# Kernel tuning notes

Measured on AMD Instinct MI355X. Metric: run time of the kernel, lower is better.

The kernel has to match this reference:

```python
import jax, jax.numpy as jnp
import numpy as np

DN = ('NCHW', 'OIHW', 'NCHW')

def _conv(x, w, b):
    y = jax.lax.conv_general_dilated(x, w, (2, 2), 'SAME', dimension_numbers=DN)
    return jax.nn.relu(y + b[None, :, None, None])

def setup_inputs() -> dict:
    key = jax.random.key(0)
    ks = jax.random.split(key, 20)
    B, S, V, D, NC = 64, 128, 32000, 512, 1000
    inp = {}
    inp['images'] = jax.random.normal(ks[0], (B, 3, 224, 224), jnp.float32)
    inp['sequences'] = jax.random.randint(ks[1], (B, S), 0, V)
    inp['lengths'] = jax.random.randint(ks[2], (B,), 1, S + 1)
    inp['lengths_var'] = inp['lengths']
    s = 0.02
    inp['emb'] = jax.random.normal(ks[3], (V, D), jnp.float32) * s
    # SimpleCNN(3): 4 strided conv blocks 3->64->128->256->512, final_dim=512
    chans = [3, 64, 128, 256, 512]
    for i in range(4):
        inp[f'cw{i+1}'] = jax.random.normal(ks[4 + i], (chans[i + 1], chans[i], 3, 3), jnp.float32) * s
        inp[f'cb{i+1}'] = jnp.zeros((chans[i + 1],), jnp.float32)
    inp['rnn_w'] = jax.random.normal(ks[8], (D, D), jnp.float32) * s
    inp['rnn_b'] = jnp.zeros((D,), jnp.float32)
    inp['fc1_w'] = jax.random.normal(ks[9], (D + 512, 512), jnp.float32) * s
    inp['fc1_b'] = jnp.zeros((512,), jnp.float32)
    inp['fc2_w'] = jax.random.normal(ks[10], (512, 512), jnp.float32) * s
    inp['fc2_b'] = jnp.zeros((512,), jnp.float32)
    inp['clf_w'] = jax.random.normal(ks[11], (512, NC), jnp.float32) * s
    inp['clf_b'] = jnp.zeros((NC,), jnp.float32)
    return inp

def reference(images, sequences, lengths, lengths_var, emb, cw1, cb1, cw2, cb2, cw3, cb3, cw4, cb4, rnn_w, rnn_b, fc1_w, fc1_b, fc2_w, fc2_b, clf_w, clf_b):
    B, S = sequences.shape
    # masked mean over valid tokens (replaces the per-sample python loop)
    we = emb[sequences]                                   # [B,S,512]
    mask = (jnp.arange(S)[None, :] < lengths[:, None]).astype(we.dtype)
    batch_means = (we * mask[:, :, None]).sum(1) / lengths.astype(we.dtype)[:, None]
    sent = batch_means @ rnn_w + rnn_b                    # [B,512]
    # SimpleCNN + global avg pool -> [B,512,1,1] -> squeeze
    x = _conv(images, cw1, cb1)
    x = _conv(x, cw2, cb2)
    x = _conv(x, cw3, cb3)
    x = _conv(x, cw4, cb4)
    img = x.mean(axis=(2, 3))                             # [B,512]
    feats = jnp.concatenate([img, sent], axis=1)          # [B,1024]
    h = jax.nn.relu(feats @ fc1_w + fc1_b)
    h = jax.nn.relu(h @ fc2_w + fc2_b)                    # dropout = identity (eval)
    return h @ clf_w + clf_b
```

## Files before the change

### kernel.cpp

```cpp
#include <hip/hip_runtime.h>
#include <hip/hip_bf16.h>
#include <cstddef>
#include <cstdint>

typedef unsigned short u16;
typedef __attribute__((ext_vector_type(8))) short bf16x8;
typedef __attribute__((ext_vector_type(4))) float f32x4;
typedef __attribute__((ext_vector_type(8))) unsigned short u16x8;

static __device__ __forceinline__ u16 f2bf(float x) {
  unsigned u = __float_as_uint(x);
  u += 0x7fffu + ((u >> 16) & 1u);
  return (u16)(u >> 16);
}
static __device__ __forceinline__ float bflo(unsigned u) { return __uint_as_float(u << 16); }
static __device__ __forceinline__ float bfhi(unsigned u) { return __uint_as_float(u & 0xffff0000u); }

static __device__ __forceinline__ void gll16(const u16* g, u16* l) {
  __builtin_amdgcn_global_load_lds(
      (const __attribute__((address_space(1))) void*)g,
      (__attribute__((address_space(3))) void*)l, 16, 0, 0);
}

static __device__ __forceinline__ void halo_store(u16* buf, int H, int W, int C,
                                                  long long i) {
  const int c8n = C >> 3;
  const int c8 = (int)(i % c8n);
  long long rem = i / c8n;
  const int p = (int)(rem % (W + 1 + H));
  const int n = (int)(rem / (W + 1 + H));
  int y, x;
  if (p <= W) { y = H; x = p; } else { y = p - (W + 1); x = W; }
  const u16x8 z = {0, 0, 0, 0, 0, 0, 0, 0};
  *(u16x8*)(buf + (((size_t)n * (H + 1) + y) * (W + 1) + x) * C + c8 * 8) = z;
}
__global__ __launch_bounds__(256) void zero_halo3(u16* __restrict__ A,
                                                  u16* __restrict__ B,
                                                  u16* __restrict__ Cb, int nimg) {
  long long i = (long long)blockIdx.x * 256 + threadIdx.x;
  const long long cA = (long long)nimg * 225 * 8;
  const long long cB = (long long)nimg * 113 * 16;
  const long long cC = (long long)nimg * 57 * 32;
  if (i < cA) { halo_store(A, 112, 112, 64, i); return; }
  i -= cA;
  if (i < cB) { halo_store(B, 56, 56, 128, i); return; }
  i -= cB;
  if (i < cC) halo_store(Cb, 28, 28, 256, i);
}

__global__ __launch_bounds__(256) void conv1_s2(
    const float* __restrict__ in,
    const float* __restrict__ w,
    const float* __restrict__ bias,
    u16* __restrict__ out) {
  __shared__ float sw[64 * 27];
  __shared__ float sb[64];
  __shared__ u16 so[256 * 64];
  const int tid = threadIdx.x;
  if (tid < 64) sb[tid] = bias[tid];
  for (int i = tid; i < 64 * 27; i += 256) sw[i] = w[i];
  __syncthreads();
  const int n = blockIdx.y;
  const int by = blockIdx.x / 7, bx = blockIdx.x % 7;
  const int oy = by * 16 + (tid >> 4), ox = bx * 16 + (tid & 15);
  const float* ibase = in + (size_t)n * 3 * 224 * 224 + (size_t)(2 * oy) * 224 + 2 * ox;
  float v[27];
  #pragma unroll
  for (int c = 0; c < 3; ++c)
    #pragma unroll
    for (int r = 0; r < 3; ++r)
      #pragma unroll
      for (int s = 0; s < 3; ++s) {
        const int iy = 2 * oy + r, ix = 2 * ox + s;
        float x = 0.f;
        if (iy < 224 && ix < 224) x = ibase[(size_t)c * 224 * 224 + r * 224 + s];
        v[c * 9 + r * 3 + s] = x;
      }
  #pragma unroll
  for (int kc = 0; kc < 8; ++kc) {
    u16x8 pack;
    #pragma unroll
    for (int k8 = 0; k8 < 8; ++k8) {
      const int k = kc * 8 + k8;
      float a = sb[k];
      const float* wk = &sw[k * 27];
      #pragma unroll
      for (int t = 0; t < 27; ++t) a = fmaf(v[t], wk[t], a);
      pack[k8] = f2bf(fmaxf(a, 0.f));
    }
    *(u16x8*)&so[(tid * 8 + (kc ^ (tid & 7))) * 8] = pack;
  }
  __syncthreads();
  u16* obase = out + (((size_t)n * 113 + by * 16) * 113 + bx * 16) * 64;
  #pragma unroll
  for (int it = 0; it < 8; ++it) {
    const int row = it * 2 + (tid >> 7);
    const int q = tid & 127;
    const int px = q >> 3, c8 = q & 7;
    const int p = row * 16 + px;
    u16x8 v8 = *(const u16x8*)&so[(p * 8 + (c8 ^ (p & 7))) * 8];
    *(u16x8*)(obase + ((size_t)row * 113 + px) * 64 + c8 * 8) = v8;
  }
}

static __device__ __forceinline__ void pack_one(const float* __restrict__ w,
                                                u16* __restrict__ pw,
                                                int CB, int NB, int C, int idx) {
  const int j = idx & 7;
  const int L = (idx >> 3) & 63;
  int t = idx >> 9;
  const int nbg = t % NB; t /= NB;
  const int cb = t % CB;
  const int tap = t / CB;
  const int n = nbg * 16 + (L & 15);
  const int c = cb * 32 + ((L >> 4) << 3) + j;
  pw[idx] = f2bf(w[((size_t)n * C + c) * 9 + tap]);
}
__global__ __launch_bounds__(256) void pack_all(
    const float* __restrict__ w2, const float* __restrict__ w3,
    const float* __restrict__ w4, u16* __restrict__ p2,
    u16* __restrict__ p3, u16* __restrict__ p4) {
  int i = blockIdx.x * 256 + threadIdx.x;
  if (i < 9 * 64 * 128) { pack_one(w2, p2, 2, 8, 64, i); return; }
  i -= 9 * 64 * 128;
  if (i < 9 * 128 * 256) { pack_one(w3, p3, 4, 16, 128, i); return; }
  i -= 9 * 128 * 256;
  if (i < 9 * 256 * 512) pack_one(w4, p4, 8, 32, 256, i);
}

template<int C, int K, int OH, int OW>
__global__ __launch_bounds__(256) void conv3x3s2_mfma(
    const u16* __restrict__ in,
    const u16* __restrict__ pw,
    const float* __restrict__ bias,
    u16* __restrict__ out) {
  constexpr int IH = 2 * OH, IW = 2 * OW;
  constexpr int PIW = IW + 1;
  constexpr int P = OH * OW;
  constexpr int BM = 128;
  constexpr int MB = (P + BM - 1) / BM;
  constexpr int CB = C / 32, NB = K / 16;
  constexpr int STEPS = 9 * CB;

  __shared__ u16 lds[2][8192];

  const int bm = blockIdx.x % MB;
  const int n = blockIdx.x / MB;
  const int nbh = blockIdx.y;
  const int lane = threadIdx.x & 63, wv = threadIdx.x >> 6;
  const int mh = wv >> 1, nh = wv & 1;

  const u16* ibase = in + (size_t)n * ((IH + 1) * PIW * C);
  int s_abase[4];
  #pragma unroll
  for (int mf = 0; mf < 4; ++mf) {
    int pm = bm * BM + mh * 64 + mf * 16 + (lane & 15);
    int pc = pm < P ? pm : P - 1;
    int oy = pc / OW, ox = pc % OW;
    s_abase[mf] = ((2 * oy) * PIW + 2 * ox) * C + ((lane >> 4) << 3);
  }

  f32x4 acc[4][4];
  #pragma unroll
  for (int mf = 0; mf < 4; ++mf)
    #pragma unroll
    for (int nf = 0; nf < 4; ++nf) acc[mf][nf] = (f32x4){0.f, 0.f, 0.f, 0.f};

  auto STAGE = [&](int st, int buf) {
    if (nh == 0) {
      const int cb = st & (CB - 1);
      const int tap = st / CB;
      const int r = tap / 3, s = tap - 3 * r;
      const int toff = (r * PIW + s) * C + cb * 32;
      #pragma unroll
      for (int mf = 0; mf < 4; ++mf)
        gll16(ibase + s_abase[mf] + toff, &lds[buf][(mh * 4 + mf) * 512]);
    } else {
      const u16* bp = pw + ((size_t)st * NB + nbh * 8 + mh * 4) * 512 + lane * 8;
      #pragma unroll
      for (int nf = 0; nf < 4; ++nf)
        gll16(bp + nf * 512, &lds[buf][4096 + (mh * 4 + nf) * 512]);
    }
  };

  STAGE(0, 0);
  __syncthreads();
  for (int st = 0; st < STEPS; ++st) {
    const int buf = st & 1;
    if (st + 1 < STEPS) STAGE(st + 1, buf ^ 1);
    bf16x8 a[4], b[4];
    #pragma unroll
    for (int mf = 0; mf < 4; ++mf)
      a[mf] = *(const bf16x8*)&lds[buf][(mh * 4 + mf) * 512 + lane * 8];
    #pragma unroll
    for (int nf = 0; nf < 4; ++nf)
      b[nf] = *(const bf16x8*)&lds[buf][4096 + (nh * 4 + nf) * 512 + lane * 8];
    #pragma unroll
    for (int mf = 0; mf < 4; ++mf)
      #pragma unroll
      for (int nf = 0; nf < 4; ++nf)
        acc[mf][nf] = __builtin_amdgcn_mfma_f32_16x16x32_bf16(a[mf], b[nf], acc[mf][nf], 0, 0, 0);
    __syncthreads();
  }

  const int rowg = (lane >> 4) << 2;
  #pragma unroll
  for (int mf = 0; mf < 4; ++mf)
    #pragma unroll
    for (int nf = 0; nf < 4; ++nf) {
      const int ch = (nbh * 8 + nh * 4 + nf) * 16 + (lane & 15);
      const float bv = bias[ch];
      #pragma unroll
      for (int rr = 0; rr < 4; ++rr) {
        const int pix = bm * BM + mh * 64 + mf * 16 + rowg + rr;
        if (pix < P) {
          const int oy = pix / OW, ox = pix % OW;
          out[(((size_t)n * (OH + 1) + oy) * (OW + 1) + ox) * K + ch] =
              f2bf(fmaxf(acc[mf][nf][rr] + bv, 0.f));
        }
      }
    }
}

__global__ __launch_bounds__(256) void avgpool_nhwc(
    const u16* __restrict__ in, float* __restrict__ feats, int n0) {
  const int n = blockIdx.x, t = threadIdx.x;
  const u16* p = in + (size_t)n * (15 * 15 * 512) + t * 2;
  float s0 = 0.f, s1 = 0.f;
  for (int y = 0; y < 14; ++y)
    #pragma unroll
    for (int x = 0; x < 14; ++x) {
      unsigned u = *(const unsigned*)(p + (size_t)(y * 15 + x) * 512);
      s0 += bflo(u);
      s1 += bfhi(u);
    }
  float* f = feats + (size_t)(n0 + n) * 1024;
  f[2 * t] = s0 * (1.f / 196.f);
  f[2 * t + 1] = s1 * (1.f / 196.f);
}

__global__ __launch_bounds__(256) void embed_mean_kernel(
    const int* __restrict__ seq, const int* __restrict__ len,
    const float* __restrict__ emb, float* __restrict__ means) {
  __shared__ float part[3][512];
  const int b = blockIdx.x;
  const int L = len[b];
  const int sg = threadIdx.x >> 6;
  const int d0 = (threadIdx.x & 63) * 8;
  float a[8] = {0.f, 0.f, 0.f, 0.f, 0.f, 0.f, 0.f, 0.f};
  for (int s = sg; s < L; s += 4) {
    const float* e = emb + (size_t)seq[b * 128 + s] * 512 + d0;
    float4 v0 = *(const float4*)e, v1 = *(const float4*)(e + 4);
    a[0] += v0.x; a[1] += v0.y; a[2] += v0.z; a[3] += v0.w;
    a[4] += v1.x; a[5] += v1.y; a[6] += v1.z; a[7] += v1.w;
  }
  if (sg) {
    #pragma unroll
    for (int j = 0; j < 8; ++j) part[sg - 1][d0 + j] = a[j];
  }
  __syncthreads();
  if (sg == 0) {
    const float inv = 1.f / (float)L;
    #pragma unroll
    for (int j = 0; j < 8; ++j)
      means[(size_t)b * 512 + d0 + j] =
          (a[j] + part[0][d0 + j] + part[1][d0 + j] + part[2][d0 + j]) * inv;
  }
}

template<int K, int N, bool RELU>
__global__ __launch_bounds__(256) void fc_kernel(
    const float* __restrict__ x, int ldx,
    const float* __restrict__ w, const float* __restrict__ bias,
    float* __restrict__ out, int ldo) {
  __shared__ float row[2][K];
  const int m0 = blockIdx.y * 2;
  for (int i = threadIdx.x; i < 2 * K; i += 256)
    row[i / K][i % K] = x[(size_t)(m0 + i / K) * ldx + (i % K)];
  __syncthreads();
  const int col = blockIdx.x * 256 + threadIdx.x;
  if (col < N) {
    float acc[2][4] = {{0.f, 0.f, 0.f, 0.f}, {0.f, 0.f, 0.f, 0.f}};
    for (int k = 0; k < K; k += 4) {
      float w0 = w[(size_t)(k + 0) * N + col];
      float w1 = w[(size_t)(k + 1) * N + col];
      float w2 = w[(size_t)(k + 2) * N + col];
      float w3 = w[(size_t)(k + 3) * N + col];
      #pragma unroll
      for (int m = 0; m < 2; ++m) {
        acc[m][0] = fmaf(row[m][k + 0], w0, acc[m][0]);
        acc[m][1] = fmaf(row[m][k + 1], w1, acc[m][1]);
        acc[m][2] = fmaf(row[m][k + 2], w2, acc[m][2]);
        acc[m][3] = fmaf(row[m][k + 3], w3, acc[m][3]);
      }
    }
    const float bv = bias[col];
    #pragma unroll
    for (int m = 0; m < 2; ++m) {
      float a = acc[m][0] + acc[m][1] + acc[m][2] + acc[m][3] + bv;
      out[(size_t)(m0 + m) * ldo + col] = RELU ? fmaxf(a, 0.f) : a;
    }
  }
}

extern "C" void kernel_launch(void* const* d_in, const int* in_sizes, int n_in,
                              void* d_out, int out_size, void* d_ws, size_t ws_size,
                              hipStream_t stream) {
  const float* images = (const float*)d_in[0];
  const int*   seq    = (const int*)d_in[1];
  const int*   len    = (const int*)d_in[2];
  const float* emb    = (const float*)d_in[4];
  const float* cw1 = (const float*)d_in[5];  const float* cb1 = (const float*)d_in[6];
  const float* cw2 = (const float*)d_in[7];  const float* cb2 = (const float*)d_in[8];
  const float* cw3 = (const float*)d_in[9];  const float* cb3 = (const float*)d_in[10];
  const float* cw4 = (const float*)d_in[11]; const float* cb4 = (const float*)d_in[12];
  const float* rnn_w = (const float*)d_in[13]; const float* rnn_b = (const float*)d_in[14];
  const float* fc1_w = (const float*)d_in[15]; const float* fc1_b = (const float*)d_in[16];
  const float* fc2_w = (const float*)d_in[17]; const float* fc2_b = (const float*)d_in[18];
  const float* clf_w = (const float*)d_in[19]; const float* clf_b = (const float*)d_in[20];
  float* out = (float*)d_out;

  const size_t A_E = (size_t)113 * 113 * 64;
  const size_t B_E = (size_t)57 * 57 * 128;
  const size_t C_E = (size_t)29 * 29 * 256;
  const size_t D_E = (size_t)15 * 15 * 512;
  const size_t PW2_E = 9 * 64 * 128, PW3_E = 9 * 128 * 256, PW4_E = 9 * 256 * 512;
  const size_t PER_IMG = (A_E + B_E + C_E + D_E) * 2;
  const size_t FIXED = (PW2_E + PW3_E + PW4_E) * 2 +
                       (size_t)(64 * 512 + 64 * 1024 + 64 * 512 + 64 * 512) * 4;
  int chunk = 64;
  if (ws_size < FIXED + 64 * PER_IMG) {
    size_t avail = (ws_size > FIXED) ? (ws_size - FIXED) : 0;
    size_t c = avail / PER_IMG;
    chunk = (c < 1) ? 1 : (c > 64 ? 64 : (int)c);
  }
  u16* bufA = (u16*)d_ws;
  u16* bufB = bufA + (size_t)chunk * A_E;
  u16* bufC = bufB + (size_t)chunk * B_E;
  u16* bufD = bufC + (size_t)chunk * C_E;
  u16* pw2 = bufD + (size_t)chunk * D_E;
  u16* pw3 = pw2 + PW2_E;
  u16* pw4 = pw3 + PW3_E;
  float* means = (float*)(pw4 + PW4_E);
  float* feats = means + 64 * 512;
  float* h1 = feats + 64 * 1024;
  float* h2 = h1 + 64 * 512;

  {
    const int pk_total = 9 * 64 * 128 + 9 * 128 * 256 + 9 * 256 * 512;
    pack_all<<<(pk_total + 255) / 256, 256, 0, stream>>>(cw2, cw3, cw4, pw2, pw3, pw4);
    long long zt = (long long)chunk * (225 * 8 + 113 * 16 + 57 * 32);
    zero_halo3<<<(int)((zt + 255) / 256), 256, 0, stream>>>(bufA, bufB, bufC, chunk);
  }

  embed_mean_kernel<<<64, 256, 0, stream>>>(seq, len, emb, means);
  fc_kernel<512, 512, false><<<dim3(2, 32), 256, 0, stream>>>(
      means, 512, rnn_w, rnn_b, feats + 512, 1024);

  for (int n0 = 0; n0 < 64; n0 += chunk) {
    int nb = 64 - n0; if (nb > chunk) nb = chunk;
    conv1_s2<<<dim3(49, nb), 256, 0, stream>>>(
        images + (size_t)n0 * 3 * 224 * 224, cw1, cb1, bufA);
    conv3x3s2_mfma<64, 128, 56, 56><<<dim3(25 * nb, 1), 256, 0, stream>>>(
        bufA, pw2, cb2, bufB);
    conv3x3s2_mfma<128, 256, 28, 28><<<dim3(7 * nb, 2), 256, 0, stream>>>(
        bufB, pw3, cb3, bufC);
    conv3x3s2_mfma<256, 512, 14, 14><<<dim3(2 * nb, 4), 256, 0, stream>>>(
        bufC, pw4, cb4, bufD);
    avgpool_nhwc<<<nb, 256, 0, stream>>>(bufD, feats, n0);
  }

  fc_kernel<1024, 512, true ><<<dim3(2, 32), 256, 0, stream>>>(feats, 1024, fc1_w, fc1_b, h1, 512);
  fc_kernel<512,  512, true ><<<dim3(2, 32), 256, 0, stream>>>(h1,    512,  fc2_w, fc2_b, h2, 512);
  fc_kernel<512, 1000, false><<<dim3(4, 32), 256, 0, stream>>>(h2,    512,  clf_w, clf_b, out, 1000);
}
```

Before: 388.2 us.

## Flatten conv M across batch, double K-step depth, and batch more FC rows

The implicit-GEMM conv now tiles the flattened batch×pixel dimension, so partial tiles at image boundaries no longer waste MFMA work. Each pipeline phase now stages two K-steps (BK=64), which halves the number of barriers but doubles LDS to 64 KB per block. The loop also gains setprio hints, explicit waitcnt/barrier scheduling, and launch_bounds(256,2). Separately, the FC kernels process four rows per block instead of two, halving redundant weight reads at the cost of fewer blocks.

```diff
diff --git a/kernel.cpp b/kernel.cpp
--- a/kernel.cpp
+++ b/kernel.cpp
@@ -129,35 +129,35 @@
 }
 
 template<int C, int K, int OH, int OW>
-__global__ __launch_bounds__(256) void conv3x3s2_mfma(
+__global__ __launch_bounds__(256, 2) void conv3x3s2_mfma(
     const u16* __restrict__ in,
     const u16* __restrict__ pw,
     const float* __restrict__ bias,
-    u16* __restrict__ out) {
+    u16* __restrict__ out,
+    int M_total) {
   constexpr int IH = 2 * OH, IW = 2 * OW;
   constexpr int PIW = IW + 1;
   constexpr int P = OH * OW;
-  constexpr int BM = 128;
-  constexpr int MB = (P + BM - 1) / BM;
   constexpr int CB = C / 32, NB = K / 16;
-  constexpr int STEPS = 9 * CB;
-
-  __shared__ u16 lds[2][8192];
-
-  const int bm = blockIdx.x % MB;
-  const int n = blockIdx.x / MB;
+  constexpr int NPH = 9 * CB / 2;
+  static_assert((9 * CB) % 2 == 0, "BK=64 needs even step count");
+
+  __shared__ u16 lds[2][16384];
+
+  const int bm = blockIdx.x;
   const int nbh = blockIdx.y;
   const int lane = threadIdx.x & 63, wv = threadIdx.x >> 6;
   const int mh = wv >> 1, nh = wv & 1;
 
-  const u16* ibase = in + (size_t)n * ((IH + 1) * PIW * C);
-  int s_abase[4];
+  int s_aoff[4];
   #pragma unroll
   for (int mf = 0; mf < 4; ++mf) {
-    int pm = bm * BM + mh * 64 + mf * 16 + (lane & 15);
-    int pc = pm < P ? pm : P - 1;
-    int oy = pc / OW, ox = pc % OW;
-    s_abase[mf] = ((2 * oy) * PIW + 2 * ox) * C + ((lane >> 4) << 3);
+    int pm = bm * 128 + mh * 64 + mf * 16 + (lane & 15);
+    if (pm >= M_total) pm = M_total - 1;
+    const int n = pm / P;
+    const int p = pm - n * P;
+    const int oy = p / OW, ox = p - oy * OW;
+    s_aoff[mf] = ((n * (IH + 1) + 2 * oy) * PIW + 2 * ox) * C + ((lane >> 4) << 3);
   }
 
   f32x4 acc[4][4];
@@ -166,41 +166,63 @@
     #pragma unroll
     for (int nf = 0; nf < 4; ++nf) acc[mf][nf] = (f32x4){0.f, 0.f, 0.f, 0.f};
 
-  auto STAGE = [&](int st, int buf) {
+  auto STAGE = [&](int ph, int buf) {
+    const int st0 = 2 * ph;
+    const int tap = st0 / CB;
+    const int cb0 = st0 & (CB - 1);
+    const int r = tap / 3, s = tap - 3 * r;
+    u16* Lb = &lds[buf][0];
     if (nh == 0) {
-      const int cb = st & (CB - 1);
-      const int tap = st / CB;
-      const int r = tap / 3, s = tap - 3 * r;
-      const int toff = (r * PIW + s) * C + cb * 32;
+      const int toff = (r * PIW + s) * C + cb0 * 32;
+      #pragma unroll
+      for (int kk = 0; kk < 2; ++kk)
+        #pragma unroll
+        for (int mf = 0; mf < 4; ++mf)
+          gll16(in + s_aoff[mf] + toff + kk * 32,
+                &Lb[(kk * 8 + mh * 4 + mf) * 512]);
+    } else {
+      const u16* bp = pw + ((size_t)(st0 + mh) * NB + nbh * 8) * 512 + lane * 8;
+      #pragma unroll
+      for (int nf = 0; nf < 8; ++nf)
+        gll16(bp + nf * 512, &Lb[8192 + (mh * 8 + nf) * 512]);
+    }
+  };
+  auto COMPUTE = [&](int buf) {
+    u16* Lb = &lds[buf][0];
+    bf16x8 a[4][2], b[4][2];
+    #pragma unroll
+    for (int kk = 0; kk < 2; ++kk) {
       #pragma unroll
       for (int mf = 0; mf < 4; ++mf)
-        gll16(ibase + s_abase[mf] + toff, &lds[buf][(mh * 4 + mf) * 512]);
-    } else {
-      const u16* bp = pw + ((size_t)st * NB + nbh * 8 + mh * 4) * 512 + lane * 8;
+        a[mf][kk] = *(const bf16x8*)&Lb[(kk * 8 + mh * 4 + mf) * 512 + lane * 8];
       #pragma unroll
       for (int nf = 0; nf < 4; ++nf)
-        gll16(bp + nf * 512, &lds[buf][4096 + (mh * 4 + nf) * 512]);
-    }
+        b[nf][kk] = *(const bf16x8*)&Lb[8192 + (kk * 8 + nh * 4 + nf) * 512 + lane * 8];
+    }
+    #pragma unroll
+    for (int kk = 0; kk < 2; ++kk)
+      #pragma unroll
+      for (int mf = 0; mf < 4; ++mf)
+        #pragma unroll
+        for (int nf = 0; nf < 4; ++nf)
+          acc[mf][nf] = __builtin_amdgcn_mfma_f32_16x16x32_bf16(
+              a[mf][kk], b[nf][kk], acc[mf][nf], 0, 0, 0);
   };
 
   STAGE(0, 0);
-  __syncthreads();
-  for (int st = 0; st < STEPS; ++st) {
-    const int buf = st & 1;
-    if (st + 1 < STEPS) STAGE(st + 1, buf ^ 1);
-    bf16x8 a[4], b[4];
-    #pragma unroll
-    for (int mf = 0; mf < 4; ++mf)
-      a[mf] = *(const bf16x8*)&lds[buf][(mh * 4 + mf) * 512 + lane * 8];
-    #pragma unroll
-    for (int nf = 0; nf < 4; ++nf)
-      b[nf] = *(const bf16x8*)&lds[buf][4096 + (nh * 4 + nf) * 512 + lane * 8];
-    #pragma unroll
-    for (int mf = 0; mf < 4; ++mf)
-      #pragma unroll
-      for (int nf = 0; nf < 4; ++nf)
-        acc[mf][nf] = __builtin_amdgcn_mfma_f32_16x16x32_bf16(a[mf], b[nf], acc[mf][nf], 0, 0, 0);
-    __syncthreads();
+  asm volatile("s_waitcnt vmcnt(0)" ::: "memory");
+  __builtin_amdgcn_s_barrier();
+  __builtin_amdgcn_sched_barrier(0);
+
+  for (int ph = 0; ph < NPH; ++ph) {
+    const int buf = ph & 1;
+    if (ph + 1 < NPH) STAGE(ph + 1, buf ^ 1);
+    __builtin_amdgcn_s_setprio(1);
+    COMPUTE(buf);
+    __builtin_amdgcn_s_setprio(0);
+    asm volatile("s_waitcnt vmcnt(0)" ::: "memory");
+    __builtin_amdgcn_s_barrier();
+    __builtin_amdgcn_sched_barrier(0);
   }
 
   const int rowg = (lane >> 4) << 2;
@@ -212,9 +234,11 @@
       const float bv = bias[ch];
       #pragma unroll
       for (int rr = 0; rr < 4; ++rr) {
-        const int pix = bm * BM + mh * 64 + mf * 16 + rowg + rr;
-        if (pix < P) {
-          const int oy = pix / OW, ox = pix % OW;
+        const int pm = bm * 128 + mh * 64 + mf * 16 + rowg + rr;
+        if (pm < M_total) {
+          const int n = pm / P;
+          const int p = pm - n * P;
+          const int oy = p / OW, ox = p - oy * OW;
           out[(((size_t)n * (OH + 1) + oy) * (OW + 1) + ox) * K + ch] =
               f2bf(fmaxf(acc[mf][nf][rr] + bv, 0.f));
         }
@@ -273,31 +297,27 @@
     const float* __restrict__ x, int ldx,
     const float* __restrict__ w, const float* __restrict__ bias,
     float* __restrict__ out, int ldo) {
-  __shared__ float row[2][K];
-  const int m0 = blockIdx.y * 2;
-  for (int i = threadIdx.x; i < 2 * K; i += 256)
+  __shared__ float row[4][K];
+  const int m0 = blockIdx.y * 4;
+  for (int i = threadIdx.x; i < 4 * K; i += 256)
     row[i / K][i % K] = x[(size_t)(m0 + i / K) * ldx + (i % K)];
   __syncthreads();
   const int col = blockIdx.x * 256 + threadIdx.x;
   if (col < N) {
-    float acc[2][4] = {{0.f, 0.f, 0.f, 0.f}, {0.f, 0.f, 0.f, 0.f}};
-    for (int k = 0; k < K; k += 4) {
+    float acc[4][2] = {{0.f, 0.f}, {0.f, 0.f}, {0.f, 0.f}, {0.f, 0.f}};
+    for (int k = 0; k < K; k += 2) {
       float w0 = w[(size_t)(k + 0) * N + col];
       float w1 = w[(size_t)(k + 1) * N + col];
-      float w2 = w[(size_t)(k + 2) * N + col];
-      float w3 = w[(size_t)(k + 3) * N + col];
-      #pragma unroll
-      for (int m = 0; m < 2; ++m) {
+      #pragma unroll
+      for (int m = 0; m < 4; ++m) {
         acc[m][0] = fmaf(row[m][k + 0], w0, acc[m][0]);
         acc[m][1] = fmaf(row[m][k + 1], w1, acc[m][1]);
-        acc[m][2] = fmaf(row[m][k + 2], w2, acc[m][2]);
-        acc[m][3] = fmaf(row[m][k + 3], w3, acc[m][3]);
       }
     }
     const float bv = bias[col];
     #pragma unroll
-    for (int m = 0; m < 2; ++m) {
-      float a = acc[m][0] + acc[m][1] + acc[m][2] + acc[m][3] + bv;
+    for (int m = 0; m < 4; ++m) {
+      float a = acc[m][0] + acc[m][1] + bv;
       out[(size_t)(m0 + m) * ldo + col] = RELU ? fmaxf(a, 0.f) : a;
     }
   }
@@ -354,23 +374,24 @@
   }
 
   embed_mean_kernel<<<64, 256, 0, stream>>>(seq, len, emb, means);
-  fc_kernel<512, 512, false><<<dim3(2, 32), 256, 0, stream>>>(
+  fc_kernel<512, 512, false><<<dim3(2, 16), 256, 0, stream>>>(
       means, 512, rnn_w, rnn_b, feats + 512, 1024);
 
   for (int n0 = 0; n0 < 64; n0 += chunk) {
     int nb = 64 - n0; if (nb > chunk) nb = chunk;
     conv1_s2<<<dim3(49, nb), 256, 0, stream>>>(
         images + (size_t)n0 * 3 * 224 * 224, cw1, cb1, bufA);
-    conv3x3s2_mfma<64, 128, 56, 56><<<dim3(25 * nb, 1), 256, 0, stream>>>(
-        bufA, pw2, cb2, bufB);
-    conv3x3s2_mfma<128, 256, 28, 28><<<dim3(7 * nb, 2), 256, 0, stream>>>(
-        bufB, pw3, cb3, bufC);
-    conv3x3s2_mfma<256, 512, 14, 14><<<dim3(2 * nb, 4), 256, 0, stream>>>(
-        bufC, pw4, cb4, bufD);
+    const int M2 = nb * 56 * 56, M3 = nb * 28 * 28, M4 = nb * 14 * 14;
+    conv3x3s2_mfma<64, 128, 56, 56><<<dim3((M2 + 127) / 128, 1), 256, 0, stream>>>(
+        bufA, pw2, cb2, bufB, M2);
+    conv3x3s2_mfma<128, 256, 28, 28><<<dim3((M3 + 127) / 128, 2), 256, 0, stream>>>(
+        bufB, pw3, cb3, bufC, M3);
+    conv3x3s2_mfma<256, 512, 14, 14><<<dim3((M4 + 127) / 128, 4), 256, 0, stream>>>(
+        bufC, pw4, cb4, bufD, M4);
     avgpool_nhwc<<<nb, 256, 0, stream>>>(bufD, feats, n0);
   }
 
-  fc_kernel<1024, 512, true ><<<dim3(2, 32), 256, 0, stream>>>(feats, 1024, fc1_w, fc1_b, h1, 512);
-  fc_kernel<512,  512, true ><<<dim3(2, 32), 256, 0, stream>>>(h1,    512,  fc2_w, fc2_b, h2, 512);
-  fc_kernel<512, 1000, false><<<dim3(4, 32), 256, 0, stream>>>(h2,    512,  clf_w, clf_b, out, 1000);
-}
+  fc_kernel<1024, 512, true ><<<dim3(2, 16), 256, 0, stream>>>(feats, 1024, fc1_w, fc1_b, h1, 512);
+  fc_kernel<512,  512, true ><<<dim3(2, 16), 256, 0, stream>>>(h1,    512,  fc2_w, fc2_b, h2, 512);
+  fc_kernel<512, 1000, false><<<dim3(4, 16), 256, 0, stream>>>(h2,    512,  clf_w, clf_b, out, 1000);
+}
```

Result: slower. 466.7 us (+20.2%).
